# Optimization experiments

Measured on AMD Instinct MI355X. Metric: run time of the kernel, lower is better.

Reference implementation:

```python
import jax, jax.numpy as jnp
import numpy as np

DIM = 256

def setup_inputs() -> dict:
    key = jax.random.key(0)
    ks = jax.random.split(key, 7)
    s = 1.0 / np.sqrt(DIM)
    x = jax.random.normal(ks[0], (16, DIM, 32, 32), dtype=jnp.float32)
    proj_w = jax.random.uniform(ks[1], (DIM, DIM), jnp.float32, -s, s)
    proj_b = jax.random.uniform(ks[2], (DIM,), jnp.float32, -s, s)
    w1 = jax.random.uniform(ks[3], (DIM, DIM), jnp.float32, -s, s)
    b1 = jax.random.uniform(ks[4], (DIM,), jnp.float32, -s, s)
    w2 = jax.random.uniform(ks[5], (DIM, DIM), jnp.float32, -s, s)
    b2 = jax.random.uniform(ks[6], (DIM,), jnp.float32, -s, s)
    return {"x": x, "proj_w": proj_w, "proj_b": proj_b, "w1": w1, "b1": b1, "w2": w2, "b2": b2}

def reference(x, proj_w, proj_b, w1, b1, w2, b2):
    B, C, H, W = x.shape
    # nodes: [B, N, C] with N = H*W
    nodes = x.reshape(B, C, H * W).transpose(0, 2, 1)
    q = nodes @ proj_w.T + proj_b                      # [B,N,C]
    scores = jnp.einsum('bnc,bmc->bnm', q, q) / jnp.sqrt(jnp.float32(C))
    attn = jax.nn.softmax(scores, axis=-1)             # [B,N,N]
    agg = jnp.einsum('bnm,bmc->bnc', attn, nodes)      # [B,N,C]
    h = jax.nn.gelu(agg @ w1.T + b1, approximate=False)
    out = h @ w2.T + b2                                # [B,N,C]
    return x + out.transpose(0, 2, 1).reshape(B, C, H, W)
```

## Files before the change

### kernel.cpp

```cpp
#include <hip/hip_runtime.h>
#include <stdint.h>

typedef unsigned short u16;
typedef __attribute__((ext_vector_type(8))) short short8;
typedef __attribute__((ext_vector_type(4))) short short4v;
typedef __attribute__((ext_vector_type(4))) float f32x4;

#define NB    16
#define DIM   256
#define NTOK  1024

__device__ __forceinline__ u16 f2b(float f) {
    union { float f; uint32_t u; } v; v.f = f;
    uint32_t u = v.u;
    u += 0x7fffu + ((u >> 16) & 1u);
    return (u16)(u >> 16);
}
__device__ __forceinline__ uint32_t pack2(float a, float b) {
    return (uint32_t)f2b(a) | ((uint32_t)f2b(b) << 16);
}
__device__ __forceinline__ f32x4 mfma16(short8 a, short8 b, f32x4 c) {
    return __builtin_amdgcn_mfma_f32_16x16x32_bf16(a, b, c, 0, 0, 0);
}
__device__ __forceinline__ f32x4 mfma16k16(short4v a, short4v b, f32x4 c) {
    asm volatile("v_mfma_f32_16x16x16_bf16 %0, %1, %2, %0"
                 : "+v"(c) : "v"(a), "v"(b));
    return c;
}
__device__ __forceinline__ short8 ld8(const u16* p) {
    return *reinterpret_cast<const short8*>(p);
}
__device__ __forceinline__ short4v ld4(const u16* p) {
    return *reinterpret_cast<const short4v*>(p);
}
__device__ __forceinline__ void gl_lds(const u16* g, u16* l) {
    __builtin_amdgcn_global_load_lds((const __attribute__((address_space(1))) void*)g,
                                     (__attribute__((address_space(3))) void*)l, 16, 0, 0);
}

__global__ __launch_bounds__(256) void pack_kernel(const float* __restrict__ x,
                                                   u16* __restrict__ xbf,
                                                   u16* __restrict__ nodes,
                                                   const float* __restrict__ pw,
                                                   const float* __restrict__ w1,
                                                   const float* __restrict__ w2,
                                                   u16* __restrict__ wbf) {
    __shared__ float tile[64][67];
    int tid = threadIdx.x;
    int blk = blockIdx.x;
    if (blk >= 1024) {
        int e = (blk - 1024) * 2048 + tid * 8;
        const float* s; int off;
        if (e < 65536)       { s = pw; off = e; }
        else if (e < 131072) { s = w1; off = e - 65536; }
        else                 { s = w2; off = e - 131072; }
        float4 f0 = *reinterpret_cast<const float4*>(s + off);
        float4 f1 = *reinterpret_cast<const float4*>(s + off + 4);
        ushort4 a, bb;
        a.x = f2b(f0.x); a.y = f2b(f0.y); a.z = f2b(f0.z); a.w = f2b(f0.w);
        bb.x = f2b(f1.x); bb.y = f2b(f1.y); bb.z = f2b(f1.z); bb.w = f2b(f1.w);
        *reinterpret_cast<ushort4*>(wbf + e)     = a;
        *reinterpret_cast<ushort4*>(wbf + e + 4) = bb;
        return;
    }
    int b  = blk >> 6;
    int t  = blk & 63;
    int c0 = (t >> 4) << 6;
    int n0 = (t & 15) << 6;
    const float* xb = x + (size_t)b * (DIM * NTOK);
    u16* xbb = xbf + (size_t)b * (DIM * NTOK);
#pragma unroll
    for (int i = 0; i < 4; i++) {
        int idx = i * 256 + tid;
        int cl = idx >> 4, nq = idx & 15;
        float4 f = *reinterpret_cast<const float4*>(xb + (size_t)(c0 + cl) * NTOK + n0 + nq * 4);
        tile[cl][nq * 4 + 0] = f.x;
        tile[cl][nq * 4 + 1] = f.y;
        tile[cl][nq * 4 + 2] = f.z;
        tile[cl][nq * 4 + 3] = f.w;
        ushort4 s;
        s.x = f2b(f.x); s.y = f2b(f.y); s.z = f2b(f.z); s.w = f2b(f.w);
        *reinterpret_cast<ushort4*>(xbb + (size_t)(c0 + cl) * NTOK + n0 + nq * 4) = s;
    }
    __syncthreads();
#pragma unroll
    for (int i = 0; i < 4; i++) {
        int idx = i * 256 + tid;
        int nl = idx >> 4, cq = idx & 15;
        ushort4 s;
        s.x = f2b(tile[cq * 4 + 0][nl]);
        s.y = f2b(tile[cq * 4 + 1][nl]);
        s.z = f2b(tile[cq * 4 + 2][nl]);
        s.w = f2b(tile[cq * 4 + 3][nl]);
        *reinterpret_cast<ushort4*>(nodes + (size_t)(b * NTOK + n0 + nl) * DIM + c0 + cq * 4) = s;
    }
}

__global__ __launch_bounds__(256) void proj_kernel(const u16* __restrict__ nodes,
                                                   const u16* __restrict__ wbf,
                                                   const float* __restrict__ pb,
                                                   u16* __restrict__ qb) {
    int lane = threadIdx.x & 63;
    int w = threadIdx.x >> 6;
    int lo = lane & 15, hi = lane >> 4;
    int ch = blockIdx.x & 3;
    int row0 = (blockIdx.x >> 2) * 64 + w * 16;
    const u16* arow = nodes + (size_t)(row0 + lo) * DIM + hi * 8;
    f32x4 acc[4];
#pragma unroll
    for (int i = 0; i < 4; i++) acc[i] = (f32x4){0.f, 0.f, 0.f, 0.f};
#pragma unroll
    for (int t = 0; t < 8; t++) {
        short8 a = ld8(arow + t * 32);
#pragma unroll
        for (int nf = 0; nf < 4; nf++) {
            short8 bfr = ld8(wbf + ((ch * 4 + nf) * 16 + lo) * DIM + t * 32 + hi * 8);
            acc[nf] = mfma16(a, bfr, acc[nf]);
        }
    }
#pragma unroll
    for (int nf = 0; nf < 4; nf++) {
        int col = (ch * 4 + nf) * 16 + lo;
        float bias = pb[col];
#pragma unroll
        for (int r = 0; r < 4; r++) {
            int row = row0 + hi * 4 + r;
            qb[(size_t)row * DIM + col] = f2b(acc[nf][r] + bias);
        }
    }
}

__global__ __launch_bounds__(256, 2) void attn_ffn_kernel(const u16* __restrict__ qb,
                                                          const u16* __restrict__ xbf,
                                                          const u16* __restrict__ wbf,
                                                          const float* __restrict__ b1,
                                                          const float* __restrict__ b2,
                                                          const float* __restrict__ x,
                                                          float* __restrict__ out) {
    __shared__ u16 kls[2][2][4096];
    __shared__ u16 vls[2][2][4096];
    __shared__ float ellX[4][16];

    int lane = threadIdx.x & 63;
    int w = threadIdx.x >> 6;
    int qsel = w >> 1, kvh = w & 1;
    int lo = lane & 15, hi = lane >> 4;
    int b  = blockIdx.x & 15;
    int qt = blockIdx.x >> 4;
    int q0 = qt * 32 + qsel * 16;
    const u16* qbb = qb  + (size_t)b * (NTOK * DIM);
    const u16* xbb = xbf + (size_t)b * (DIM * NTOK);
    const u16* w1b = wbf + 65536;
    const u16* w2b = wbf + 131072;

    int kOff[4], vOff[4], kDst[4], vDst[4];
#pragma unroll
    for (int i = 0; i < 4; i++) {
        int kr = qsel * 8 + i * 2 + (lane >> 5);
        kOff[i] = kr * DIM + ((lane & 31) ^ (kr & 7)) * 8;
        kDst[i] = (qsel * 8 + i * 2) * 256;
        int vc = qsel * 128 + i * 32 + (lane >> 1);
        vOff[i] = vc * NTOK + (lane & 1) * 8;
        vDst[i] = (qsel * 128 + i * 32) * 16;
    }
    int kvbeg = kvh * 512;

    short8 bq[8];
#pragma unroll
    for (int t = 0; t < 8; t++)
        bq[t] = ld8(qbb + (size_t)(q0 + lo) * DIM + t * 32 + hi * 8);

    f32x4 acc[16];
#pragma unroll
    for (int i = 0; i < 16; i++) acc[i] = (f32x4){0.f, 0.f, 0.f, 0.f};
    float ellp = 0.f;
    const float C1 = 0.0625f * 1.44269504f;
    const float OFF = 12.0f;

#pragma unroll
    for (int i = 0; i < 4; i++) {
        gl_lds(qbb + kvbeg * DIM + kOff[i], &kls[kvh][0][kDst[i]]);
        gl_lds(xbb + kvbeg       + vOff[i], &vls[kvh][0][vDst[i]]);
    }
    __syncthreads();

    for (int tt = 0; tt < 32; tt++) {
        int buf = tt & 1;
        if (tt < 31) {
            int base = kvbeg + (tt + 1) * 16;
#pragma unroll
            for (int i = 0; i < 4; i++) {
                gl_lds(qbb + base * DIM + kOff[i], &kls[kvh][buf ^ 1][kDst[i]]);
                gl_lds(xbb + base       + vOff[i], &vls[kvh][buf ^ 1][vDst[i]]);
            }
        }
        const u16* kb = &kls[kvh][buf][0];
        const u16* vb = &vls[kvh][buf][0];

        f32x4 sa = (f32x4){0.f, 0.f, 0.f, 0.f};
        f32x4 sb = (f32x4){0.f, 0.f, 0.f, 0.f};
        __builtin_amdgcn_s_setprio(1);
#pragma unroll
        for (int t = 0; t < 8; t += 2) {
            int sl0 = ((t * 4 + hi) ^ (lo & 7)) * 8;
            int sl1 = (((t + 1) * 4 + hi) ^ (lo & 7)) * 8;
            sa = mfma16(ld8(kb + lo * 256 + sl0), bq[t],     sa);
            sb = mfma16(ld8(kb + lo * 256 + sl1), bq[t + 1], sb);
        }
        __builtin_amdgcn_s_setprio(0);

        float p0 = exp2f((sa[0] + sb[0]) * C1 - OFF);
        float p1 = exp2f((sa[1] + sb[1]) * C1 - OFF);
        float p2 = exp2f((sa[2] + sb[2]) * C1 - OFF);
        float p3 = exp2f((sa[3] + sb[3]) * C1 - OFF);
        ellp += (p0 + p1) + (p2 + p3);

        union { uint32_t u[2]; short4v v; } pa;
        pa.u[0] = pack2(p0, p1);
        pa.u[1] = pack2(p2, p3);

        __builtin_amdgcn_s_setprio(1);
#pragma unroll
        for (int mf = 0; mf < 16; mf++) {
            short4v vf = ld4(vb + (mf * 16 + lo) * 16 + hi * 4);
            acc[mf] = mfma16k16(vf, pa.v, acc[mf]);
        }
        __builtin_amdgcn_s_setprio(0);
        __syncthreads();
    }

    asm volatile("s_nop 7\n\ts_nop 7" ::: "memory");

    float e = ellp;
    e += __shfl_xor(e, 16);
    e += __shfl_xor(e, 32);
    if (lane < 16) ellX[w][lane] = e;

    char* pbase = (char*)kls;
    if (kvh == 0) {
#pragma unroll
        for (int j = 0; j < 8; j++) {
            int byt = w * 8192 + lo * 512 + ((j * 64 + hi * 16) ^ ((lo & 7) << 4));
            *reinterpret_cast<f32x4*>(pbase + byt) = acc[8 + j];
        }
    } else {
#pragma unroll
        for (int j = 0; j < 8; j++) {
            int byt = w * 8192 + lo * 512 + ((j * 64 + hi * 16) ^ ((lo & 7) << 4));
            *reinterpret_cast<f32x4*>(pbase + byt) = acc[j];
        }
    }
    __syncthreads();
    float rinv = 1.f / (e + ellX[w ^ 1][lo]);
    char* abase = (char*)vls;
    int arow = qsel * 16 + lo;
    if (kvh == 0) {
#pragma unroll
        for (int j = 0; j < 8; j++) {
            int byt = (w ^ 1) * 8192 + lo * 512 + ((j * 64 + hi * 16) ^ ((lo & 7) << 4));
            f32x4 o = *reinterpret_cast<const f32x4*>(pbase + byt);
            uint32_t lo32 = pack2((acc[j][0] + o[0]) * rinv, (acc[j][1] + o[1]) * rinv);
            uint32_t hi32 = pack2((acc[j][2] + o[2]) * rinv, (acc[j][3] + o[3]) * rinv);
            int slot = j * 2 + (hi >> 1);
            int byteA = arow * 512 + ((slot ^ (lo & 7)) * 16) + (hi & 1) * 8;
            *reinterpret_cast<uint32_t*>(abase + byteA)     = lo32;
            *reinterpret_cast<uint32_t*>(abase + byteA + 4) = hi32;
        }
    } else {
#pragma unroll
        for (int j = 0; j < 8; j++) {
            int byt = (w ^ 1) * 8192 + lo * 512 + ((j * 64 + hi * 16) ^ ((lo & 7) << 4));
            f32x4 o = *reinterpret_cast<const f32x4*>(pbase + byt);
            uint32_t lo32 = pack2((acc[8 + j][0] + o[0]) * rinv, (acc[8 + j][1] + o[1]) * rinv);
            uint32_t hi32 = pack2((acc[8 + j][2] + o[2]) * rinv, (acc[8 + j][3] + o[3]) * rinv);
            int slot = 16 + j * 2 + (hi >> 1);
            int byteA = arow * 512 + ((slot ^ (lo & 7)) * 16) + (hi & 1) * 8;
            *reinterpret_cast<uint32_t*>(abase + byteA)     = lo32;
            *reinterpret_cast<uint32_t*>(abase + byteA + 4) = hi32;
        }
    }
    __syncthreads();

    int rh = w & 1, chh = w >> 1;
    f32x4 f1[8];
#pragma unroll
    for (int i = 0; i < 8; i++) f1[i] = (f32x4){0.f, 0.f, 0.f, 0.f};
#pragma unroll
    for (int t = 0; t < 8; t++) {
        int g = ((t * 4 + hi) ^ (lo & 7)) * 16;
        short8 a = *reinterpret_cast<const short8*>(abase + (rh * 16 + lo) * 512 + g);
#pragma unroll
        for (int nf = 0; nf < 8; nf++) {
            short8 bfr = ld8(w1b + ((chh * 8 + nf) * 16 + lo) * DIM + t * 32 + hi * 8);
            f1[nf] = mfma16(a, bfr, f1[nf]);
        }
    }
    u16* hl = (u16*)kls;
#pragma unroll
    for (int nf = 0; nf < 8; nf++) {
        int f = (chh * 8 + nf) * 16 + lo;
        float bias = b1[f];
#pragma unroll
        for (int r = 0; r < 4; r++) {
            float v = f1[nf][r] + bias;
            float g = 0.5f * v * (1.f + erff(v * 0.70710678f));
            hl[(rh * 16 + hi * 4 + r) * 264 + f] = f2b(g);
        }
    }
    __syncthreads();

    f32x4 f2[8];
#pragma unroll
    for (int i = 0; i < 8; i++) f2[i] = (f32x4){0.f, 0.f, 0.f, 0.f};
#pragma unroll
    for (int t = 0; t < 8; t++) {
        short8 bh = ld8(hl + (rh * 16 + lo) * 264 + t * 32 + hi * 8);
#pragma unroll
        for (int mf = 0; mf < 8; mf++) {
            short8 a2 = ld8(w2b + ((chh * 8 + mf) * 16 + lo) * DIM + t * 32 + hi * 8);
            f2[mf] = mfma16(a2, bh, f2[mf]);
        }
    }
    int n = qt * 32 + rh * 16 + lo;
#pragma unroll
    for (int mf = 0; mf < 8; mf++) {
#pragma unroll
        for (int r = 0; r < 4; r++) {
            int co = (chh * 8 + mf) * 16 + hi * 4 + r;
            size_t addr = (size_t)b * (DIM * NTOK) + (size_t)co * NTOK + n;
            out[addr] = f2[mf][r] + b2[co] + x[addr];
        }
    }
}

extern "C" void kernel_launch(void* const* d_in, const int* in_sizes, int n_in,
                              void* d_out, int out_size, void* d_ws, size_t ws_size,
                              hipStream_t stream) {
    const float* x      = (const float*)d_in[0];
    const float* proj_w = (const float*)d_in[1];
    const float* proj_b = (const float*)d_in[2];
    const float* w1     = (const float*)d_in[3];
    const float* b1     = (const float*)d_in[4];
    const float* w2     = (const float*)d_in[5];
    const float* b2     = (const float*)d_in[6];
    float* out = (float*)d_out;

    u16* xbf   = (u16*)d_ws;
    u16* nodes = xbf   + 4194304;
    u16* qb    = nodes + 4194304;
    u16* wbf   = qb    + 4194304;

    pack_kernel    <<<1120, 256, 0, stream>>>(x, xbf, nodes, proj_w, w1, w2, wbf);
    proj_kernel    <<<1024, 256, 0, stream>>>(nodes, wbf, proj_b, qb);
    attn_ffn_kernel<<<512,  256, 0, stream>>>(qb, xbf, wbf, b1, b2, x, out);
}
```

Baseline: 117.7 us.

## Fuse pack and projection kernels, load V directly from global in attention

```diff
diff --git a/kernel.cpp b/kernel.cpp
--- a/kernel.cpp
+++ b/kernel.cpp
@@ -3,7 +3,6 @@
 
 typedef unsigned short u16;
 typedef __attribute__((ext_vector_type(8))) short short8;
-typedef __attribute__((ext_vector_type(4))) short short4v;
 typedef __attribute__((ext_vector_type(4))) float f32x4;
 
 #define NB    16
@@ -22,110 +21,101 @@
 __device__ __forceinline__ f32x4 mfma16(short8 a, short8 b, f32x4 c) {
     return __builtin_amdgcn_mfma_f32_16x16x32_bf16(a, b, c, 0, 0, 0);
 }
-__device__ __forceinline__ f32x4 mfma16k16(short4v a, short4v b, f32x4 c) {
-    asm volatile("v_mfma_f32_16x16x16_bf16 %0, %1, %2, %0"
-                 : "+v"(c) : "v"(a), "v"(b));
-    return c;
-}
 __device__ __forceinline__ short8 ld8(const u16* p) {
     return *reinterpret_cast<const short8*>(p);
-}
-__device__ __forceinline__ short4v ld4(const u16* p) {
-    return *reinterpret_cast<const short4v*>(p);
 }
 __device__ __forceinline__ void gl_lds(const u16* g, u16* l) {
     __builtin_amdgcn_global_load_lds((const __attribute__((address_space(1))) void*)g,
                                      (__attribute__((address_space(3))) void*)l, 16, 0, 0);
 }
 
-__global__ __launch_bounds__(256) void pack_kernel(const float* __restrict__ x,
-                                                   u16* __restrict__ xbf,
-                                                   u16* __restrict__ nodes,
-                                                   const float* __restrict__ pw,
-                                                   const float* __restrict__ w1,
-                                                   const float* __restrict__ w2,
-                                                   u16* __restrict__ wbf) {
-    __shared__ float tile[64][67];
+__global__ __launch_bounds__(256) void wconv_kernel(const float* __restrict__ pw,
+                                                    const float* __restrict__ w1,
+                                                    const float* __restrict__ w2,
+                                                    u16* __restrict__ wbf) {
+    int e = blockIdx.x * 2048 + threadIdx.x * 8;
+    const float* s; int off;
+    if (e < 65536)       { s = pw; off = e; }
+    else if (e < 131072) { s = w1; off = e - 65536; }
+    else                 { s = w2; off = e - 131072; }
+    float4 f0 = *reinterpret_cast<const float4*>(s + off);
+    float4 f1 = *reinterpret_cast<const float4*>(s + off + 4);
+    ushort4 a, b;
+    a.x = f2b(f0.x); a.y = f2b(f0.y); a.z = f2b(f0.z); a.w = f2b(f0.w);
+    b.x = f2b(f1.x); b.y = f2b(f1.y); b.z = f2b(f1.z); b.w = f2b(f1.w);
+    *reinterpret_cast<ushort4*>(wbf + e)     = a;
+    *reinterpret_cast<ushort4*>(wbf + e + 4) = b;
+}
+
+__global__ __launch_bounds__(256) void packproj_kernel(const float* __restrict__ x,
+                                                       u16* __restrict__ xbf,
+                                                       const u16* __restrict__ wbf,
+                                                       const float* __restrict__ pb,
+                                                       u16* __restrict__ qb) {
+    __shared__ float stage[64][68];
+    __shared__ u16 tile[64 * 256];
     int tid = threadIdx.x;
-    int blk = blockIdx.x;
-    if (blk >= 1024) {
-        int e = (blk - 1024) * 2048 + tid * 8;
-        const float* s; int off;
-        if (e < 65536)       { s = pw; off = e; }
-        else if (e < 131072) { s = w1; off = e - 65536; }
-        else                 { s = w2; off = e - 131072; }
-        float4 f0 = *reinterpret_cast<const float4*>(s + off);
-        float4 f1 = *reinterpret_cast<const float4*>(s + off + 4);
-        ushort4 a, bb;
-        a.x = f2b(f0.x); a.y = f2b(f0.y); a.z = f2b(f0.z); a.w = f2b(f0.w);
-        bb.x = f2b(f1.x); bb.y = f2b(f1.y); bb.z = f2b(f1.z); bb.w = f2b(f1.w);
-        *reinterpret_cast<ushort4*>(wbf + e)     = a;
-        *reinterpret_cast<ushort4*>(wbf + e + 4) = bb;
-        return;
-    }
-    int b  = blk >> 6;
-    int t  = blk & 63;
-    int c0 = (t >> 4) << 6;
-    int n0 = (t & 15) << 6;
+    int lane = tid & 63;
+    int w = tid >> 6;
+    int lo = lane & 15, hi = lane >> 4;
+    int b  = blockIdx.x & 15;
+    int nt = blockIdx.x >> 4;
+    int n0 = nt * 64;
     const float* xb = x + (size_t)b * (DIM * NTOK);
     u16* xbb = xbf + (size_t)b * (DIM * NTOK);
-#pragma unroll
-    for (int i = 0; i < 4; i++) {
-        int idx = i * 256 + tid;
-        int cl = idx >> 4, nq = idx & 15;
-        float4 f = *reinterpret_cast<const float4*>(xb + (size_t)(c0 + cl) * NTOK + n0 + nq * 4);
-        tile[cl][nq * 4 + 0] = f.x;
-        tile[cl][nq * 4 + 1] = f.y;
-        tile[cl][nq * 4 + 2] = f.z;
-        tile[cl][nq * 4 + 3] = f.w;
-        ushort4 s;
-        s.x = f2b(f.x); s.y = f2b(f.y); s.z = f2b(f.z); s.w = f2b(f.w);
-        *reinterpret_cast<ushort4*>(xbb + (size_t)(c0 + cl) * NTOK + n0 + nq * 4) = s;
-    }
-    __syncthreads();
-#pragma unroll
-    for (int i = 0; i < 4; i++) {
-        int idx = i * 256 + tid;
-        int nl = idx >> 4, cq = idx & 15;
-        ushort4 s;
-        s.x = f2b(tile[cq * 4 + 0][nl]);
-        s.y = f2b(tile[cq * 4 + 1][nl]);
-        s.z = f2b(tile[cq * 4 + 2][nl]);
-        s.w = f2b(tile[cq * 4 + 3][nl]);
-        *reinterpret_cast<ushort4*>(nodes + (size_t)(b * NTOK + n0 + nl) * DIM + c0 + cq * 4) = s;
-    }
-}
-
-__global__ __launch_bounds__(256) void proj_kernel(const u16* __restrict__ nodes,
-                                                   const u16* __restrict__ wbf,
-                                                   const float* __restrict__ pb,
-                                                   u16* __restrict__ qb) {
-    int lane = threadIdx.x & 63;
-    int w = threadIdx.x >> 6;
-    int lo = lane & 15, hi = lane >> 4;
-    int ch = blockIdx.x & 3;
-    int row0 = (blockIdx.x >> 2) * 64 + w * 16;
-    const u16* arow = nodes + (size_t)(row0 + lo) * DIM + hi * 8;
-    f32x4 acc[4];
-#pragma unroll
-    for (int i = 0; i < 4; i++) acc[i] = (f32x4){0.f, 0.f, 0.f, 0.f};
+
+#pragma unroll
+    for (int cc = 0; cc < 4; cc++) {
+#pragma unroll
+        for (int i = 0; i < 4; i++) {
+            int idx = i * 256 + tid;
+            int cl = idx >> 4, nq = idx & 15;
+            float4 f = *reinterpret_cast<const float4*>(
+                xb + (size_t)(cc * 64 + cl) * NTOK + n0 + nq * 4);
+            stage[cl][nq * 4 + 0] = f.x;
+            stage[cl][nq * 4 + 1] = f.y;
+            stage[cl][nq * 4 + 2] = f.z;
+            stage[cl][nq * 4 + 3] = f.w;
+            ushort4 s;
+            s.x = f2b(f.x); s.y = f2b(f.y); s.z = f2b(f.z); s.w = f2b(f.w);
+            *reinterpret_cast<ushort4*>(xbb + (size_t)(cc * 64 + cl) * NTOK + n0 + nq * 4) = s;
+        }
+        __syncthreads();
+#pragma unroll
+        for (int j = 0; j < 2; j++) {
+            int item = j * 256 + tid;
+            int nl = item >> 3, g = item & 7;
+            union { u16 s[8]; short8 v; } o;
+#pragma unroll
+            for (int k = 0; k < 8; k++) o.s[k] = f2b(stage[g * 8 + k][nl]);
+            int gi = (cc * 8 + g) ^ (nl & 7);
+            *reinterpret_cast<short8*>(&tile[nl * 256 + gi * 8]) = o.v;
+        }
+        __syncthreads();
+    }
+
+    f32x4 acc[16];
+#pragma unroll
+    for (int i = 0; i < 16; i++) acc[i] = (f32x4){0.f, 0.f, 0.f, 0.f};
+    int ar = w * 16 + lo;
 #pragma unroll
     for (int t = 0; t < 8; t++) {
-        short8 a = ld8(arow + t * 32);
-#pragma unroll
-        for (int nf = 0; nf < 4; nf++) {
-            short8 bfr = ld8(wbf + ((ch * 4 + nf) * 16 + lo) * DIM + t * 32 + hi * 8);
+        int gi = (t * 4 + hi) ^ (lo & 7);
+        short8 a = ld8(&tile[ar * 256 + gi * 8]);
+#pragma unroll
+        for (int nf = 0; nf < 16; nf++) {
+            short8 bfr = ld8(wbf + (nf * 16 + lo) * DIM + t * 32 + hi * 8);
             acc[nf] = mfma16(a, bfr, acc[nf]);
         }
     }
 #pragma unroll
-    for (int nf = 0; nf < 4; nf++) {
-        int col = (ch * 4 + nf) * 16 + lo;
+    for (int nf = 0; nf < 16; nf++) {
+        int col = nf * 16 + lo;
         float bias = pb[col];
 #pragma unroll
         for (int r = 0; r < 4; r++) {
-            int row = row0 + hi * 4 + r;
-            qb[(size_t)row * DIM + col] = f2b(acc[nf][r] + bias);
+            int row = n0 + w * 16 + hi * 4 + r;
+            qb[(size_t)(b * NTOK + row) * DIM + col] = f2b(acc[nf][r] + bias);
         }
     }
 }
@@ -137,8 +127,7 @@
                                                           const float* __restrict__ b2,
                                                           const float* __restrict__ x,
                                                           float* __restrict__ out) {
-    __shared__ u16 kls[2][2][4096];
-    __shared__ u16 vls[2][2][4096];
+    __shared__ u16 kls[2][2][8192];
     __shared__ float ellX[4][16];
 
     int lane = threadIdx.x & 63;
@@ -153,15 +142,12 @@
     const u16* w1b = wbf + 65536;
     const u16* w2b = wbf + 131072;
 
-    int kOff[4], vOff[4], kDst[4], vDst[4];
-#pragma unroll
-    for (int i = 0; i < 4; i++) {
-        int kr = qsel * 8 + i * 2 + (lane >> 5);
+    int kOff[8], kDst[8];
+#pragma unroll
+    for (int i = 0; i < 8; i++) {
+        int kr = qsel * 16 + i * 2 + (lane >> 5);
         kOff[i] = kr * DIM + ((lane & 31) ^ (kr & 7)) * 8;
-        kDst[i] = (qsel * 8 + i * 2) * 256;
-        int vc = qsel * 128 + i * 32 + (lane >> 1);
-        vOff[i] = vc * NTOK + (lane & 1) * 8;
-        vDst[i] = (qsel * 128 + i * 32) * 16;
+        kDst[i] = (qsel * 16 + i * 2) * 256;
     }
     int kvbeg = kvh * 512;
 
@@ -178,58 +164,68 @@
     const float OFF = 12.0f;
 
 #pragma unroll
-    for (int i = 0; i < 4; i++) {
+    for (int i = 0; i < 8; i++)
         gl_lds(qbb + kvbeg * DIM + kOff[i], &kls[kvh][0][kDst[i]]);
-        gl_lds(xbb + kvbeg       + vOff[i], &vls[kvh][0][vDst[i]]);
-    }
     __syncthreads();
 
-    for (int tt = 0; tt < 32; tt++) {
+    for (int tt = 0; tt < 16; tt++) {
         int buf = tt & 1;
-        if (tt < 31) {
-            int base = kvbeg + (tt + 1) * 16;
-#pragma unroll
-            for (int i = 0; i < 4; i++) {
-                gl_lds(qbb + base * DIM + kOff[i], &kls[kvh][buf ^ 1][kDst[i]]);
-                gl_lds(xbb + base       + vOff[i], &vls[kvh][buf ^ 1][vDst[i]]);
-            }
+        int kv0 = kvbeg + tt * 32;
+        if (tt < 15) {
+#pragma unroll
+            for (int i = 0; i < 8; i++)
+                gl_lds(qbb + (kv0 + 32) * DIM + kOff[i], &kls[kvh][buf ^ 1][kDst[i]]);
         }
         const u16* kb = &kls[kvh][buf][0];
-        const u16* vb = &vls[kvh][buf][0];
-
-        f32x4 sa = (f32x4){0.f, 0.f, 0.f, 0.f};
-        f32x4 sb = (f32x4){0.f, 0.f, 0.f, 0.f};
+
+        f32x4 s0a = (f32x4){0.f,0.f,0.f,0.f}, s0b = (f32x4){0.f,0.f,0.f,0.f};
+        f32x4 s1a = (f32x4){0.f,0.f,0.f,0.f}, s1b = (f32x4){0.f,0.f,0.f,0.f};
         __builtin_amdgcn_s_setprio(1);
 #pragma unroll
         for (int t = 0; t < 8; t += 2) {
             int sl0 = ((t * 4 + hi) ^ (lo & 7)) * 8;
             int sl1 = (((t + 1) * 4 + hi) ^ (lo & 7)) * 8;
-            sa = mfma16(ld8(kb + lo * 256 + sl0), bq[t],     sa);
-            sb = mfma16(ld8(kb + lo * 256 + sl1), bq[t + 1], sb);
+            s0a = mfma16(ld8(kb + lo * 256 + sl0),        bq[t],     s0a);
+            s0b = mfma16(ld8(kb + lo * 256 + sl1),        bq[t + 1], s0b);
+            s1a = mfma16(ld8(kb + (16 + lo) * 256 + sl0), bq[t],     s1a);
+            s1b = mfma16(ld8(kb + (16 + lo) * 256 + sl1), bq[t + 1], s1b);
         }
         __builtin_amdgcn_s_setprio(0);
 
-        float p0 = exp2f((sa[0] + sb[0]) * C1 - OFF);
-        float p1 = exp2f((sa[1] + sb[1]) * C1 - OFF);
-        float p2 = exp2f((sa[2] + sb[2]) * C1 - OFF);
-        float p3 = exp2f((sa[3] + sb[3]) * C1 - OFF);
-        ellp += (p0 + p1) + (p2 + p3);
-
-        union { uint32_t u[2]; short4v v; } pa;
-        pa.u[0] = pack2(p0, p1);
-        pa.u[1] = pack2(p2, p3);
-
+        float p0[4], p1[4];
+#pragma unroll
+        for (int r = 0; r < 4; r++) {
+            p0[r] = exp2f((s0a[r] + s0b[r]) * C1 - OFF);
+            p1[r] = exp2f((s1a[r] + s1b[r]) * C1 - OFF);
+            ellp += p0[r] + p1[r];
+        }
+
+        uint32_t pl0 = pack2(p0[0], p0[1]), ph0 = pack2(p0[2], p0[3]);
+        uint32_t pl1 = pack2(p1[0], p1[1]), ph1 = pack2(p1[2], p1[3]);
+        int srcA = ((hi & 1) << 5) | lo;
+        int srcB = srcA + 16;
+        uint32_t w0a = __shfl(pl0, srcA), w0b = __shfl(pl1, srcA);
+        uint32_t w1a = __shfl(ph0, srcA), w1b = __shfl(ph1, srcA);
+        uint32_t w2a = __shfl(pl0, srcB), w2b = __shfl(pl1, srcB);
+        uint32_t w3a = __shfl(ph0, srcB), w3b = __shfl(ph1, srcB);
+        bool sel = (hi >= 2);
+        union { uint32_t u[4]; short8 v; } pu;
+        pu.u[0] = sel ? w0b : w0a;
+        pu.u[1] = sel ? w1b : w1a;
+        pu.u[2] = sel ? w2b : w2a;
+        pu.u[3] = sel ? w3b : w3a;
+        short8 pfrag = pu.v;
+
+        const u16* vp = xbb + kv0 + hi * 8;
         __builtin_amdgcn_s_setprio(1);
 #pragma unroll
         for (int mf = 0; mf < 16; mf++) {
-            short4v vf = ld4(vb + (mf * 16 + lo) * 16 + hi * 4);
-            acc[mf] = mfma16k16(vf, pa.v, acc[mf]);
+            short8 a = ld8(vp + (size_t)(mf * 16 + lo) * NTOK);
+            acc[mf] = mfma16(a, pfrag, acc[mf]);
         }
         __builtin_amdgcn_s_setprio(0);
         __syncthreads();
     }
-
-    asm volatile("s_nop 7\n\ts_nop 7" ::: "memory");
 
     float e = ellp;
     e += __shfl_xor(e, 16);
@@ -252,7 +248,7 @@
     }
     __syncthreads();
     float rinv = 1.f / (e + ellX[w ^ 1][lo]);
-    char* abase = (char*)vls;
+    char* abase = (char*)kls + 32768;
     int arow = qsel * 16 + lo;
     if (kvh == 0) {
 #pragma unroll
@@ -345,12 +341,11 @@
     const float* b2     = (const float*)d_in[6];
     float* out = (float*)d_out;
 
-    u16* xbf   = (u16*)d_ws;
-    u16* nodes = xbf   + 4194304;
-    u16* qb    = nodes + 4194304;
-    u16* wbf   = qb    + 4194304;
-
-    pack_kernel    <<<1120, 256, 0, stream>>>(x, xbf, nodes, proj_w, w1, w2, wbf);
-    proj_kernel    <<<1024, 256, 0, stream>>>(nodes, wbf, proj_b, qb);
+    u16* xbf = (u16*)d_ws;
+    u16* qb  = xbf + 4194304;
+    u16* wbf = qb  + 4194304;
+
+    wconv_kernel   <<<96,   256, 0, stream>>>(proj_w, w1, w2, wbf);
+    packproj_kernel<<<256,  256, 0, stream>>>(x, xbf, wbf, proj_b, qb);
     attn_ffn_kernel<<<512,  256, 0, stream>>>(qb, xbf, wbf, b1, b2, x, out);
 }
```

New measurement: 147.3 us. +25.1%, slower.
